# Optimization experiments

Hardware: AMD Instinct MI355X
Metric: run time of the kernel (lower is better)

## Reference

```python
import jax, jax.numpy as jnp
import numpy as np
import math

B, S, D = 4, 2048, 1024

def setup_inputs() -> dict:
    key = jax.random.key(0)
    ks = jax.random.split(key, 8)
    scale = 1.0 / math.sqrt(D)
    x = jax.random.normal(ks[0], (B, S, D), dtype=jnp.float32)
    # additive causal mask: 0 on/below diag, -1e9 above (broadcast over batch)
    causal = jnp.where(jnp.tril(jnp.ones((S, S), dtype=bool)), 0.0, -1e9).astype(jnp.float32)
    mask = jnp.broadcast_to(causal, (B, S, S))
    Wq = jax.random.uniform(ks[1], (D, D), jnp.float32, -scale, scale)
    bq = jax.random.uniform(ks[2], (D,), jnp.float32, -scale, scale)
    Wk = jax.random.uniform(ks[3], (D, D), jnp.float32, -scale, scale)
    bk = jax.random.uniform(ks[4], (D,), jnp.float32, -scale, scale)
    Wv = jax.random.uniform(ks[5], (D, D), jnp.float32, -scale, scale)
    bv = jax.random.uniform(ks[6], (D,), jnp.float32, -scale, scale)
    return {"x": x, "mask": mask, "Wq": Wq, "bq": bq, "Wk": Wk, "bk": bk, "Wv": Wv, "bv": bv}

def reference(x, mask, Wq, bq, Wk, bk, Wv, bv):
    q = jnp.einsum('bsd,de->bse', x, Wq) + bq
    k = jnp.einsum('bsd,de->bse', x, Wk) + bk
    v = jnp.einsum('bsd,de->bse', x, Wv) + bv
    scores = jnp.einsum('bqd,bkd->bqk', q, k) / math.sqrt(k.shape[-1])
    attn = jax.nn.softmax(scores + mask, axis=-1)
    return jnp.einsum('bqk,bkd->bqd', attn, v)
```

## Files before the change

kernel.cpp:

```cpp
#include <hip/hip_runtime.h>
#include <hip/hip_bf16.h>
#include <hip/hip_fp16.h>
#include <math.h>

typedef short v8s __attribute__((ext_vector_type(8)));
typedef short v4s __attribute__((ext_vector_type(4)));
typedef float v4f __attribute__((ext_vector_type(4)));
typedef unsigned short ushort_t;

__device__ __forceinline__ unsigned short f2bf(float f) {
    unsigned int u = __float_as_uint(f);
    u = (u + 0x7FFFu + ((u >> 16) & 1u)) >> 16;
    return (unsigned short)u;
}
__device__ __forceinline__ unsigned short f2h(float f) {
    __half h = __float2half(f);
    return *reinterpret_cast<unsigned short*>(&h);
}
__device__ __forceinline__ float h2f(unsigned short u) {
    __half h = *reinterpret_cast<__half*>(&u);
    return __half2float(h);
}

__device__ __forceinline__ void load_lds16(const void* g, void* l) {
    __builtin_amdgcn_global_load_lds((const __attribute__((address_space(1))) void*)g,
                                     (__attribute__((address_space(3))) void*)l,
                                     16, 0, 0);
}

#define FENCE() asm volatile("" ::: "memory")
#define BAR() do { FENCE(); __builtin_amdgcn_s_barrier(); FENCE(); } while (0)

__global__ __launch_bounds__(256) void cvt_kernel(const float4* __restrict__ in,
                                                  ushort_t* __restrict__ out, int n4) {
    int i = blockIdx.x * 256 + threadIdx.x;
    int stride = gridDim.x * 256;
    for (; i < n4; i += stride) {
        float4 v = in[i];
        v4s p;
        p[0] = (short)f2bf(v.x); p[1] = (short)f2bf(v.y);
        p[2] = (short)f2bf(v.z); p[3] = (short)f2bf(v.w);
        *(v4s*)(out + (size_t)i * 4) = p;
    }
}

__global__ void transpose_w(const float* __restrict__ W0, const float* __restrict__ W1,
                            const float* __restrict__ W2, ushort_t* __restrict__ WtAll) {
    const float* W = (blockIdx.z == 0) ? W0 : (blockIdx.z == 1 ? W1 : W2);
    ushort_t* out = WtAll + (size_t)blockIdx.z * 1024 * 1024;
    __shared__ float tile[32][33];
    int n0 = blockIdx.x * 32, k0 = blockIdx.y * 32;
    int tx = threadIdx.x, ty = threadIdx.y;
    #pragma unroll
    for (int i = 0; i < 32; i += 8)
        tile[ty + i][tx] = W[(size_t)(k0 + ty + i) * 1024 + n0 + tx];
    __syncthreads();
    #pragma unroll
    for (int i = 0; i < 32; i += 8)
        out[(size_t)(n0 + ty + i) * 1024 + k0 + tx] = f2bf(tile[tx][ty + i]);
}

template <int MODE>
__global__ __launch_bounds__(MODE == 3 ? 256 : 512)
void gemm_ring(const ushort_t* __restrict__ A, int lda, long long strideA,
               const ushort_t* __restrict__ Bt, int ldb, long long strideB,
               const float* __restrict__ bq, const float* __restrict__ bk,
               const float* __restrict__ bv,
               ushort_t* __restrict__ Qb, ushort_t* __restrict__ Kb,
               ushort_t* __restrict__ Vt,
               void* __restrict__ Cv, int ldc, long long strideC, int K)
{
    constexpr int THREADS = (MODE == 3) ? 256 : 512;
    constexpr int BN      = (MODE == 3) ? 128 : 256;
    constexpr int NW      = THREADS / 64;
    constexpr int RPL     = THREADS / 4;
    constexpr int ALINES  = 128 / RPL;
    constexpr int BLINES  = BN / RPL;
    constexpr int LOADS   = ALINES + BLINES;

    int bx, by, bz = 0;
    int f = blockIdx.x;
    if constexpr (MODE == 0) {
        int xcd = f & 7, i = f >> 3;
        by = xcd * 8 + i / 12;
        bx = i % 12;
    } else if constexpr (MODE == 2) {
        int swz = (f & 7) * 36 + (f >> 3);
        bz = swz / 72; int t = swz % 72;
        int r = 0, c = 0;
        while (c + (r / 2 + 1) <= t) { c += r / 2 + 1; ++r; }
        by = r; bx = t - c;
    } else {
        int swz = (f & 7) * 64 + (f >> 3);
        bz = swz >> 7; int rem = swz & 127;
        by = 15 - (rem >> 3); bx = rem & 7;
    }

    const int tid = threadIdx.x;
    const int lane = tid & 63, wid = tid >> 6;
    const int wm = (NW == 8) ? (wid >> 2) : (wid >> 1);
    const int wc = wid & ((NW == 8) ? 3 : 1);

    const ushort_t* Ab = A + (size_t)bz * strideA;
    const ushort_t* Bb = Bt + (size_t)bz * strideB;

    __shared__ ushort_t As[3][128 * 32];
    __shared__ ushort_t Bs[3][BN * 32];

    const int brow = by * 128, bcol = bx * BN;

    int kEnd = K;
    if constexpr (MODE == 3) { int lim = (by + 1) * 128; kEnd = lim < K ? lim : K; }
    const int nt = kEnd / 32;

    v4f acc[4][4];
    #pragma unroll
    for (int mi = 0; mi < 4; ++mi)
        #pragma unroll
        for (int ni = 0; ni < 4; ++ni)
            acc[mi][ni] = (v4f)0.f;

    const int rr = tid >> 2, slot = tid & 3;
    auto STAGE = [&](int buf, int t) {
        const int k0 = t * 32;
        #pragma unroll
        for (int c = 0; c < ALINES; ++c) {
            int r = c * RPL + rr;
            int sc = ((slot ^ ((r >> 1) & 3)) << 3);
            load_lds16(Ab + (size_t)(brow + r) * lda + k0 + sc,
                       &As[buf][(size_t)(c * RPL + wid * 16) * 32]);
        }
        #pragma unroll
        for (int c = 0; c < BLINES; ++c) {
            int r = c * RPL + rr;
            int sc = ((slot ^ ((r >> 1) & 3)) << 3);
            load_lds16(Bb + (size_t)(bcol + r) * ldb + k0 + sc,
                       &Bs[buf][(size_t)(c * RPL + wid * 16) * 32]);
        }
    };

    const int frow = lane & 15, fq4 = lane >> 4;
    const int csw = ((fq4 ^ ((frow >> 1) & 3)) << 3);

    STAGE(0, 0);
    if (nt > 1) STAGE(1, 1);

    int cur = 0;
    for (int t = 0; t < nt; ++t) {
        if (t + 1 < nt) {
            asm volatile("s_waitcnt vmcnt(%0)" :: "i"(LOADS) : "memory");
        } else {
            asm volatile("s_waitcnt vmcnt(0)" ::: "memory");
        }
        BAR();
        if (t + 2 < nt) {
            int tgt = cur ? cur - 1 : 2;
            STAGE(tgt, t + 2);
        }
        const ushort_t* Ac = &As[cur][0];
        const ushort_t* Bc = &Bs[cur][0];
        v8s a[4], b[4];
        #pragma unroll
        for (int mi = 0; mi < 4; ++mi)
            a[mi] = *(const v8s*)(Ac + (size_t)(wm * 64 + mi * 16 + frow) * 32 + csw);
        #pragma unroll
        for (int ni = 0; ni < 4; ++ni)
            b[ni] = *(const v8s*)(Bc + (size_t)(wc * 64 + ni * 16 + frow) * 32 + csw);
        __builtin_amdgcn_s_setprio(1);
        #pragma unroll
        for (int mi = 0; mi < 4; ++mi)
            #pragma unroll
            for (int ni = 0; ni < 4; ++ni)
                acc[mi][ni] = __builtin_amdgcn_mfma_f32_16x16x32_bf16(a[mi], b[ni], acc[mi][ni], 0, 0, 0);
        __builtin_amdgcn_s_setprio(0);
        cur = (cur == 2) ? 0 : cur + 1;
    }

    const int fr = lane & 15;
    const int fq = lane >> 4;

    if constexpr (MODE == 0) {
        const int route = bx >> 2;
        const int cbase = (bx & 3) * 256 + wc * 64;
        if (route < 2) {
            ushort_t* C = route ? Kb : Qb;
            const float* bias = route ? bk : bq;
            const float scale = route ? 1.0f : 0.03125f;
            #pragma unroll
            for (int ni = 0; ni < 4; ++ni) {
                int cg = cbase + ni * 16 + fr;
                float bb = bias[cg];
                #pragma unroll
                for (int mi = 0; mi < 4; ++mi) {
                    int gr0 = brow + wm * 64 + mi * 16 + fq * 4;
                    #pragma unroll
                    for (int j = 0; j < 4; ++j)
                        C[(size_t)(gr0 + j) * 1024 + cg] = f2bf((acc[mi][ni][j] + bb) * scale);
                }
            }
        } else {
            #pragma unroll
            for (int ni = 0; ni < 4; ++ni) {
                int e = cbase + ni * 16 + fr;
                float bb = bv[e];
                #pragma unroll
                for (int mi = 0; mi < 4; ++mi) {
                    int gr0 = brow + wm * 64 + mi * 16 + fq * 4;
                    int bbat = gr0 >> 11;
                    int sl2 = gr0 & 2047;
                    alignas(8) ushort_t tmp[4];
                    #pragma unroll
                    for (int j = 0; j < 4; ++j)
                        tmp[j] = f2bf(acc[mi][ni][j] + bb);
                    *(v4s*)(Vt + (size_t)bbat * (1024 * 2048) + (size_t)e * 2048 + sl2) =
                        *(const v4s*)tmp;
                }
            }
        }
    } else if constexpr (MODE == 2) {
        ushort_t* C = (ushort_t*)Cv + (size_t)bz * strideC;
        #pragma unroll
        for (int ni = 0; ni < 4; ++ni) {
            int gc = bcol + wc * 64 + ni * 16 + fr;
            #pragma unroll
            for (int mi = 0; mi < 4; ++mi) {
                int gr0 = brow + wm * 64 + mi * 16 + fq * 4;
                #pragma unroll
                for (int j = 0; j < 4; ++j)
                    C[(size_t)(gr0 + j) * ldc + gc] = f2h(acc[mi][ni][j]);
            }
        }
    } else {
        float* C = (float*)Cv + (size_t)bz * strideC;
        #pragma unroll
        for (int ni = 0; ni < 4; ++ni) {
            int gc = bcol + wc * 64 + ni * 16 + fr;
            #pragma unroll
            for (int mi = 0; mi < 4; ++mi) {
                int gr0 = brow + wm * 64 + mi * 16 + fq * 4;
                #pragma unroll
                for (int j = 0; j < 4; ++j)
                    C[(size_t)(gr0 + j) * ldc + gc] = acc[mi][ni][j];
            }
        }
    }
}

__global__ __launch_bounds__(256) void softmax_causal(ushort_t* __restrict__ Sc) {
    int row = blockIdx.x;
    int b = row >> 11, i = row & 2047;
    ushort_t* srow = Sc + ((size_t)b * 2048 + i) * 2048;
    const int L = i + 1;
    const int Lw = ((i >> 7) + 1) << 7;
    __shared__ float vals[2048];
    __shared__ float red[8];
    int tid = threadIdx.x, lane = tid & 63, wid = tid >> 6;

    float mx = -3.0e38f;
    const int L4 = L >> 2;
    for (int j4 = tid; j4 < L4; j4 += 256) {
        v4s u = *(const v4s*)(srow + j4 * 4);
        float4 v;
        v.x = h2f((unsigned short)u[0]); v.y = h2f((unsigned short)u[1]);
        v.z = h2f((unsigned short)u[2]); v.w = h2f((unsigned short)u[3]);
        ((float4*)vals)[j4] = v;
        mx = fmaxf(fmaxf(mx, fmaxf(v.x, v.y)), fmaxf(v.z, v.w));
    }
    {
        int j = (L4 << 2) + tid;
        if (j < L) { float v = h2f(srow[j]); vals[j] = v; mx = fmaxf(mx, v); }
    }
    #pragma unroll
    for (int o = 32; o; o >>= 1) mx = fmaxf(mx, __shfl_down(mx, o));
    if (lane == 0) red[wid] = mx;
    __syncthreads();
    mx = fmaxf(fmaxf(red[0], red[1]), fmaxf(red[2], red[3]));

    float sum = 0.f;
    for (int j = tid; j < L; j += 256) {
        float e = __expf(vals[j] - mx);
        vals[j] = e;
        sum += e;
    }
    #pragma unroll
    for (int o = 32; o; o >>= 1) sum += __shfl_down(sum, o);
    if (lane == 0) red[wid + 4] = sum;
    __syncthreads();
    float inv = 1.f / (red[4] + red[5] + red[6] + red[7]);

    for (int j4 = tid; j4 * 4 < Lw; j4 += 256) {
        int j = j4 * 4;
        float4 v = ((const float4*)vals)[j4];
        v4s p;
        p[0] = (short)f2bf((j     < L) ? v.x * inv : 0.f);
        p[1] = (short)f2bf((j + 1 < L) ? v.y * inv : 0.f);
        p[2] = (short)f2bf((j + 2 < L) ? v.z * inv : 0.f);
        p[3] = (short)f2bf((j + 3 < L) ? v.w * inv : 0.f);
        *(v4s*)(srow + j) = p;
    }
}

extern "C" void kernel_launch(void* const* d_in, const int* in_sizes, int n_in,
                              void* d_out, int out_size, void* d_ws, size_t ws_size,
                              hipStream_t stream) {
    const float* x  = (const float*)d_in[0];
    const float* Wq = (const float*)d_in[2];
    const float* bq = (const float*)d_in[3];
    const float* Wk = (const float*)d_in[4];
    const float* bk = (const float*)d_in[5];
    const float* Wv = (const float*)d_in[6];
    const float* bv = (const float*)d_in[7];

    ushort_t* xb = (ushort_t*)d_ws;
    ushort_t* Wt = xb + (size_t)8192 * 1024;
    ushort_t* Qb = Wt + (size_t)3 * 1024 * 1024;
    ushort_t* Kb = Qb + (size_t)8192 * 1024;
    ushort_t* Vt = Kb + (size_t)8192 * 1024;
    ushort_t* Sc = Vt + (size_t)8192 * 1024;

    cvt_kernel<<<2048, 256, 0, stream>>>((const float4*)x, xb, 8192 * 1024 / 4);
    transpose_w<<<dim3(32, 32, 3), dim3(32, 8), 0, stream>>>(Wq, Wk, Wv, Wt);

    gemm_ring<0><<<768, 512, 0, stream>>>(xb, 1024, 0, Wt, 1024, 0,
                                          bq, bk, bv, Qb, Kb, Vt,
                                          nullptr, 0, 0, 1024);

    gemm_ring<2><<<288, 512, 0, stream>>>(Qb, 1024, 2048LL * 1024,
                                          Kb, 1024, 2048LL * 1024,
                                          nullptr, nullptr, nullptr,
                                          nullptr, nullptr, nullptr,
                                          Sc, 2048, 2048LL * 2048, 1024);

    softmax_causal<<<8192, 256, 0, stream>>>(Sc);

    gemm_ring<3><<<512, 256, 0, stream>>>(Sc, 2048, 2048LL * 2048,
                                          Vt, 2048, 2048LL * 1024,
                                          nullptr, nullptr, nullptr,
                                          nullptr, nullptr, nullptr,
                                          d_out, 1024, 2048LL * 1024, 2048);
    (void)in_sizes; (void)n_in; (void)out_size; (void)ws_size;
}
```

Baseline: 177.8 us.

## Add 256x256 QKV GEMM kernel, fuse prep kernels, one-wave-per-row softmax

```diff
diff --git a/kernel.cpp b/kernel.cpp
--- a/kernel.cpp
+++ b/kernel.cpp
@@ -30,44 +30,180 @@
 
 #define FENCE() asm volatile("" ::: "memory")
 #define BAR() do { FENCE(); __builtin_amdgcn_s_barrier(); FENCE(); } while (0)
-
-__global__ __launch_bounds__(256) void cvt_kernel(const float4* __restrict__ in,
-                                                  ushort_t* __restrict__ out, int n4) {
-    int i = blockIdx.x * 256 + threadIdx.x;
-    int stride = gridDim.x * 256;
-    for (; i < n4; i += stride) {
-        float4 v = in[i];
-        v4s p;
-        p[0] = (short)f2bf(v.x); p[1] = (short)f2bf(v.y);
-        p[2] = (short)f2bf(v.z); p[3] = (short)f2bf(v.w);
-        *(v4s*)(out + (size_t)i * 4) = p;
-    }
-}
-
-__global__ void transpose_w(const float* __restrict__ W0, const float* __restrict__ W1,
-                            const float* __restrict__ W2, ushort_t* __restrict__ WtAll) {
-    const float* W = (blockIdx.z == 0) ? W0 : (blockIdx.z == 1 ? W1 : W2);
-    ushort_t* out = WtAll + (size_t)blockIdx.z * 1024 * 1024;
-    __shared__ float tile[32][33];
-    int n0 = blockIdx.x * 32, k0 = blockIdx.y * 32;
-    int tx = threadIdx.x, ty = threadIdx.y;
+#define LGKM0() asm volatile("s_waitcnt lgkmcnt(0)" ::: "memory")
+#define VMC(n) asm volatile("s_waitcnt vmcnt(" #n ")" ::: "memory")
+
+__global__ __launch_bounds__(256)
+void prep_kernel(const float4* __restrict__ x4, ushort_t* __restrict__ xb,
+                 const float* __restrict__ W0, const float* __restrict__ W1,
+                 const float* __restrict__ W2, ushort_t* __restrict__ Wt) {
+    if (blockIdx.x < 2048) {
+        int i = blockIdx.x * 256 + threadIdx.x;
+        #pragma unroll
+        for (int it = 0; it < 4; ++it, i += 524288) {
+            float4 v = x4[i];
+            v4s p;
+            p[0] = (short)f2bf(v.x); p[1] = (short)f2bf(v.y);
+            p[2] = (short)f2bf(v.z); p[3] = (short)f2bf(v.w);
+            *(v4s*)(xb + (size_t)i * 4) = p;
+        }
+    } else {
+        int f = blockIdx.x - 2048;
+        int z = f >> 10; int rem = f & 1023;
+        int n0 = (rem & 31) * 32, k0 = (rem >> 5) * 32;
+        const float* W = (z == 0) ? W0 : (z == 1 ? W1 : W2);
+        ushort_t* out = Wt + (size_t)z * 1024 * 1024;
+        __shared__ float tile[32][33];
+        int tx = threadIdx.x & 31, ty = threadIdx.x >> 5;
+        #pragma unroll
+        for (int i2 = 0; i2 < 32; i2 += 8)
+            tile[ty + i2][tx] = W[(size_t)(k0 + ty + i2) * 1024 + n0 + tx];
+        __syncthreads();
+        #pragma unroll
+        for (int i2 = 0; i2 < 32; i2 += 8)
+            out[(size_t)(n0 + ty + i2) * 1024 + k0 + tx] = f2bf(tile[tx][ty + i2]);
+    }
+}
+
+__global__ __launch_bounds__(512)
+void gemm8_qkv(const ushort_t* __restrict__ A, const ushort_t* __restrict__ Bt,
+               const float* __restrict__ bq, const float* __restrict__ bk,
+               const float* __restrict__ bv,
+               ushort_t* __restrict__ Qb, ushort_t* __restrict__ Kb,
+               ushort_t* __restrict__ Vt)
+{
+    int f = blockIdx.x;
+    int xcd = f & 7, i = f >> 3;
+    const int by = xcd * 4 + i / 12;
+    const int bx = i % 12;
+
+    const int tid = threadIdx.x;
+    const int lane = tid & 63, wid = tid >> 6;
+    const int wm = wid >> 2, wc = wid & 3;
+    const int frow = lane & 15, fq4 = lane >> 4;
+
+    const int brow = by * 256, bcol = bx * 256;
+
+    __shared__ ushort_t LA[2][2][256 * 32];
+    __shared__ ushort_t LB[2][2][256 * 32];
+
+    v4f acc[8][4];
     #pragma unroll
-    for (int i = 0; i < 32; i += 8)
-        tile[ty + i][tx] = W[(size_t)(k0 + ty + i) * 1024 + n0 + tx];
-    __syncthreads();
-    #pragma unroll
-    for (int i = 0; i < 32; i += 8)
-        out[(size_t)(n0 + ty + i) * 1024 + k0 + tx] = f2bf(tile[tx][ty + i]);
+    for (int mi = 0; mi < 8; ++mi)
+        #pragma unroll
+        for (int ni = 0; ni < 4; ++ni)
+            acc[mi][ni] = (v4f)0.f;
+
+    const int srr = tid >> 2, sch = tid & 3;
+    auto ST = [&](ushort_t* dst, const ushort_t* src, int grow0, int t, int kh) {
+        #pragma unroll
+        for (int c = 0; c < 2; ++c) {
+            int r = c * 128 + srr;
+            int ch = sch ^ ((r >> 1) & 3);
+            load_lds16(src + (size_t)(grow0 + r) * 1024 + t * 64 + kh * 32 + ch * 8,
+                       dst + (size_t)(c * 128 + srr) * 32 + sch * 8);
+        }
+    };
+
+    v8s a[4], b[4];
+    const int rsw = fq4 ^ ((frow >> 1) & 3);
+    auto RDA = [&](int buf, int kh, int mh) {
+        #pragma unroll
+        for (int i2 = 0; i2 < 4; ++i2) {
+            int r = wm * 128 + (mh * 4 + i2) * 16 + frow;
+            a[i2] = *(const v8s*)(&LA[buf][kh][(size_t)r * 32 + rsw * 8]);
+        }
+    };
+    auto RDB = [&](int buf, int kh) {
+        #pragma unroll
+        for (int i2 = 0; i2 < 4; ++i2) {
+            int r = wc * 64 + i2 * 16 + frow;
+            b[i2] = *(const v8s*)(&LB[buf][kh][(size_t)r * 32 + rsw * 8]);
+        }
+    };
+    auto MM = [&](int mh) {
+        __builtin_amdgcn_s_setprio(1);
+        #pragma unroll
+        for (int i2 = 0; i2 < 4; ++i2)
+            #pragma unroll
+            for (int n = 0; n < 4; ++n)
+                acc[mh * 4 + i2][n] =
+                    __builtin_amdgcn_mfma_f32_16x16x32_bf16(a[i2], b[n], acc[mh * 4 + i2][n], 0, 0, 0);
+        __builtin_amdgcn_s_setprio(0);
+    };
+
+    ST(LA[0][0], A, brow, 0, 0); ST(LB[0][0], Bt, bcol, 0, 0);
+    ST(LA[0][1], A, brow, 0, 1); ST(LB[0][1], Bt, bcol, 0, 1);
+    ST(LA[1][0], A, brow, 1, 0); ST(LB[1][0], Bt, bcol, 1, 0);
+    VMC(4); BAR();
+
+    for (int u = 0; u < 8; ++u) {
+        const int t0 = 2 * u, t1 = 2 * u + 1;
+        const bool pf = (u < 7);
+        RDA(0, 0, 0); RDB(0, 0); ST(LA[1][1], A, brow, t1, 1);
+        BAR(); LGKM0(); MM(0); BAR();
+        RDA(0, 0, 1); ST(LB[1][1], Bt, bcol, t1, 1);
+        BAR(); LGKM0(); MM(1); BAR();
+        RDA(0, 1, 0); RDB(0, 1); if (pf) ST(LA[0][0], A, brow, t0 + 2, 0);
+        BAR(); LGKM0(); MM(0); BAR();
+        RDA(0, 1, 1); if (pf) { ST(LB[0][0], Bt, bcol, t0 + 2, 0); VMC(4); }
+        else VMC(0);
+        BAR(); LGKM0(); MM(1); BAR();
+        RDA(1, 0, 0); RDB(1, 0); if (pf) ST(LA[0][1], A, brow, t0 + 2, 1);
+        BAR(); LGKM0(); MM(0); BAR();
+        RDA(1, 0, 1); if (pf) ST(LB[0][1], Bt, bcol, t0 + 2, 1);
+        BAR(); LGKM0(); MM(1); BAR();
+        RDA(1, 1, 0); RDB(1, 1); if (pf) ST(LA[1][0], A, brow, t1 + 2, 0);
+        BAR(); LGKM0(); MM(0); BAR();
+        RDA(1, 1, 1); if (pf) { ST(LB[1][0], Bt, bcol, t1 + 2, 0); VMC(4); }
+        BAR(); LGKM0(); MM(1); BAR();
+    }
+
+    const int fr = lane & 15;
+    const int fq = lane >> 4;
+    const int route = bx >> 2;
+    const int cbase = (bx & 3) * 256 + wc * 64;
+    if (route < 2) {
+        ushort_t* C = route ? Kb : Qb;
+        const float* bias = route ? bk : bq;
+        const float scale = route ? 1.0f : 0.03125f;
+        #pragma unroll
+        for (int ni = 0; ni < 4; ++ni) {
+            int cg = cbase + ni * 16 + fr;
+            float bb = bias[cg];
+            #pragma unroll
+            for (int mi = 0; mi < 8; ++mi) {
+                int gr0 = brow + wm * 128 + mi * 16 + fq * 4;
+                #pragma unroll
+                for (int j = 0; j < 4; ++j)
+                    C[(size_t)(gr0 + j) * 1024 + cg] = f2bf((acc[mi][ni][j] + bb) * scale);
+            }
+        }
+    } else {
+        #pragma unroll
+        for (int ni = 0; ni < 4; ++ni) {
+            int e = cbase + ni * 16 + fr;
+            float bb = bv[e];
+            #pragma unroll
+            for (int mi = 0; mi < 8; ++mi) {
+                int gr0 = brow + wm * 128 + mi * 16 + fq * 4;
+                int bbat = gr0 >> 11;
+                int sl2 = gr0 & 2047;
+                alignas(8) ushort_t tmp[4];
+                #pragma unroll
+                for (int j = 0; j < 4; ++j)
+                    tmp[j] = f2bf(acc[mi][ni][j] + bb);
+                *(v4s*)(Vt + (size_t)bbat * (1024 * 2048) + (size_t)e * 2048 + sl2) =
+                    *(const v4s*)tmp;
+            }
+        }
+    }
 }
 
 template <int MODE>
 __global__ __launch_bounds__(MODE == 3 ? 256 : 512)
 void gemm_ring(const ushort_t* __restrict__ A, int lda, long long strideA,
                const ushort_t* __restrict__ Bt, int ldb, long long strideB,
-               const float* __restrict__ bq, const float* __restrict__ bk,
-               const float* __restrict__ bv,
-               ushort_t* __restrict__ Qb, ushort_t* __restrict__ Kb,
-               ushort_t* __restrict__ Vt,
                void* __restrict__ Cv, int ldc, long long strideC, int K)
 {
     constexpr int THREADS = (MODE == 3) ? 256 : 512;
@@ -78,13 +214,9 @@
     constexpr int BLINES  = BN / RPL;
     constexpr int LOADS   = ALINES + BLINES;
 
-    int bx, by, bz = 0;
+    int bx, by, bz;
     int f = blockIdx.x;
-    if constexpr (MODE == 0) {
-        int xcd = f & 7, i = f >> 3;
-        by = xcd * 8 + i / 12;
-        bx = i % 12;
-    } else if constexpr (MODE == 2) {
+    if constexpr (MODE == 2) {
         int swz = (f & 7) * 36 + (f >> 3);
         bz = swz / 72; int t = swz % 72;
         int r = 0, c = 0;
@@ -178,46 +310,7 @@
 
     const int fr = lane & 15;
     const int fq = lane >> 4;
-
-    if constexpr (MODE == 0) {
-        const int route = bx >> 2;
-        const int cbase = (bx & 3) * 256 + wc * 64;
-        if (route < 2) {
-            ushort_t* C = route ? Kb : Qb;
-            const float* bias = route ? bk : bq;
-            const float scale = route ? 1.0f : 0.03125f;
-            #pragma unroll
-            for (int ni = 0; ni < 4; ++ni) {
-                int cg = cbase + ni * 16 + fr;
-                float bb = bias[cg];
-                #pragma unroll
-                for (int mi = 0; mi < 4; ++mi) {
-                    int gr0 = brow + wm * 64 + mi * 16 + fq * 4;
-                    #pragma unroll
-                    for (int j = 0; j < 4; ++j)
-                        C[(size_t)(gr0 + j) * 1024 + cg] = f2bf((acc[mi][ni][j] + bb) * scale);
-                }
-            }
-        } else {
-            #pragma unroll
-            for (int ni = 0; ni < 4; ++ni) {
-                int e = cbase + ni * 16 + fr;
-                float bb = bv[e];
-                #pragma unroll
-                for (int mi = 0; mi < 4; ++mi) {
-                    int gr0 = brow + wm * 64 + mi * 16 + fq * 4;
-                    int bbat = gr0 >> 11;
-                    int sl2 = gr0 & 2047;
-                    alignas(8) ushort_t tmp[4];
-                    #pragma unroll
-                    for (int j = 0; j < 4; ++j)
-                        tmp[j] = f2bf(acc[mi][ni][j] + bb);
-                    *(v4s*)(Vt + (size_t)bbat * (1024 * 2048) + (size_t)e * 2048 + sl2) =
-                        *(const v4s*)tmp;
-                }
-            }
-        }
-    } else if constexpr (MODE == 2) {
+    if constexpr (MODE == 2) {
         ushort_t* C = (ushort_t*)Cv + (size_t)bz * strideC;
         #pragma unroll
         for (int ni = 0; ni < 4; ++ni) {
@@ -247,55 +340,50 @@
 }
 
 __global__ __launch_bounds__(256) void softmax_causal(ushort_t* __restrict__ Sc) {
-    int row = blockIdx.x;
-    int b = row >> 11, i = row & 2047;
+    __shared__ float vals[4][2048];
+    const int wid = threadIdx.x >> 6, lane = threadIdx.x & 63;
+    const int row = blockIdx.x * 4 + wid;
+    const int b = row >> 11, i = row & 2047;
     ushort_t* srow = Sc + ((size_t)b * 2048 + i) * 2048;
     const int L = i + 1;
     const int Lw = ((i >> 7) + 1) << 7;
-    __shared__ float vals[2048];
-    __shared__ float red[8];
-    int tid = threadIdx.x, lane = tid & 63, wid = tid >> 6;
+    float* v = vals[wid];
 
     float mx = -3.0e38f;
     const int L4 = L >> 2;
-    for (int j4 = tid; j4 < L4; j4 += 256) {
+    for (int j4 = lane; j4 < L4; j4 += 64) {
         v4s u = *(const v4s*)(srow + j4 * 4);
-        float4 v;
-        v.x = h2f((unsigned short)u[0]); v.y = h2f((unsigned short)u[1]);
-        v.z = h2f((unsigned short)u[2]); v.w = h2f((unsigned short)u[3]);
-        ((float4*)vals)[j4] = v;
-        mx = fmaxf(fmaxf(mx, fmaxf(v.x, v.y)), fmaxf(v.z, v.w));
+        float4 w;
+        w.x = h2f((unsigned short)u[0]); w.y = h2f((unsigned short)u[1]);
+        w.z = h2f((unsigned short)u[2]); w.w = h2f((unsigned short)u[3]);
+        ((float4*)v)[j4] = w;
+        mx = fmaxf(fmaxf(mx, fmaxf(w.x, w.y)), fmaxf(w.z, w.w));
     }
     {
-        int j = (L4 << 2) + tid;
-        if (j < L) { float v = h2f(srow[j]); vals[j] = v; mx = fmaxf(mx, v); }
+        int j = (L4 << 2) + lane;
+        if (j < L) { float t = h2f(srow[j]); v[j] = t; mx = fmaxf(mx, t); }
     }
     #pragma unroll
-    for (int o = 32; o; o >>= 1) mx = fmaxf(mx, __shfl_down(mx, o));
-    if (lane == 0) red[wid] = mx;
-    __syncthreads();
-    mx = fmaxf(fmaxf(red[0], red[1]), fmaxf(red[2], red[3]));
+    for (int o = 32; o; o >>= 1) mx = fmaxf(mx, __shfl_xor(mx, o));
 
     float sum = 0.f;
-    for (int j = tid; j < L; j += 256) {
-        float e = __expf(vals[j] - mx);
-        vals[j] = e;
+    for (int j = lane; j < L; j += 64) {
+        float e = __expf(v[j] - mx);
+        v[j] = e;
         sum += e;
     }
     #pragma unroll
-    for (int o = 32; o; o >>= 1) sum += __shfl_down(sum, o);
-    if (lane == 0) red[wid + 4] = sum;
-    __syncthreads();
-    float inv = 1.f / (red[4] + red[5] + red[6] + red[7]);
-
-    for (int j4 = tid; j4 * 4 < Lw; j4 += 256) {
+    for (int o = 32; o; o >>= 1) sum += __shfl_xor(sum, o);
+    float inv = 1.f / sum;
+
+    for (int j4 = lane; j4 * 4 < Lw; j4 += 64) {
         int j = j4 * 4;
-        float4 v = ((const float4*)vals)[j4];
+        float4 w = ((const float4*)v)[j4];
         v4s p;
-        p[0] = (short)f2bf((j     < L) ? v.x * inv : 0.f);
-        p[1] = (short)f2bf((j + 1 < L) ? v.y * inv : 0.f);
-        p[2] = (short)f2bf((j + 2 < L) ? v.z * inv : 0.f);
-        p[3] = (short)f2bf((j + 3 < L) ? v.w * inv : 0.f);
+        p[0] = (short)f2bf((j     < L) ? w.x * inv : 0.f);
+        p[1] = (short)f2bf((j + 1 < L) ? w.y * inv : 0.f);
+        p[2] = (short)f2bf((j + 2 < L) ? w.z * inv : 0.f);
+        p[3] = (short)f2bf((j + 3 < L) ? w.w * inv : 0.f);
         *(v4s*)(srow + j) = p;
     }
 }
@@ -318,25 +406,18 @@
     ushort_t* Vt = Kb + (size_t)8192 * 1024;
     ushort_t* Sc = Vt + (size_t)8192 * 1024;
 
-    cvt_kernel<<<2048, 256, 0, stream>>>((const float4*)x, xb, 8192 * 1024 / 4);
-    transpose_w<<<dim3(32, 32, 3), dim3(32, 8), 0, stream>>>(Wq, Wk, Wv, Wt);
-
-    gemm_ring<0><<<768, 512, 0, stream>>>(xb, 1024, 0, Wt, 1024, 0,
-                                          bq, bk, bv, Qb, Kb, Vt,
-                                          nullptr, 0, 0, 1024);
+    prep_kernel<<<5120, 256, 0, stream>>>((const float4*)x, xb, Wq, Wk, Wv, Wt);
+
+    gemm8_qkv<<<384, 512, 0, stream>>>(xb, Wt, bq, bk, bv, Qb, Kb, Vt);
 
     gemm_ring<2><<<288, 512, 0, stream>>>(Qb, 1024, 2048LL * 1024,
                                           Kb, 1024, 2048LL * 1024,
-                                          nullptr, nullptr, nullptr,
-                                          nullptr, nullptr, nullptr,
                                           Sc, 2048, 2048LL * 2048, 1024);
 
-    softmax_causal<<<8192, 256, 0, stream>>>(Sc);
+    softmax_causal<<<2048, 256, 0, stream>>>(Sc);
 
     gemm_ring<3><<<512, 256, 0, stream>>>(Sc, 2048, 2048LL * 2048,
                                           Vt, 2048, 2048LL * 1024,
-                                          nullptr, nullptr, nullptr,
-                                          nullptr, nullptr, nullptr,
                                           d_out, 1024, 2048LL * 1024, 2048);
     (void)in_sizes; (void)n_in; (void)out_size; (void)ws_size;
 }
```

New measurement: 178.3 us. About the same (+0.2%).
